# Performance work log

Measured on AMD Instinct MI355X. Metric: run time of the kernel, lower is better.

Reference implementation:

```python
import jax, jax.numpy as jnp
import numpy as np

L, H, D, F = 4, 8, 64, 256  # layers, heads, head_dim, FAVOR feature dims (n_dims=256 in source)
DM = H * D                   # d_model = 512
EPS = 1e-6                   # fast_transformers LinearAttention eps


def _ln(x, g, b):
    m = jnp.mean(x, -1, keepdims=True)
    v = jnp.mean((x - m) ** 2, -1, keepdims=True)
    return (x - m) * jax.lax.rsqrt(v + 1e-5) * g + b


def _favor(x, omega):
    # FAVOR+ softmax-kernel feature map. x: [B,S,H,D], omega: [D, F//2]
    x = x * (D ** -0.25)  # x * sqrt(softmax_temp), softmax_temp = 1/sqrt(D)
    u = jnp.einsum('bshd,df->bshf', x, omega)
    h = jnp.sum(x * x, -1, keepdims=True) * 0.5
    return jnp.concatenate([jnp.exp(u - h), jnp.exp(-u - h)], -1) * (F ** -0.5)


def _forward(x, pos, enc_w1, enc_b1, enc_w2, enc_b2, enc_g, enc_b,
             wq, bq, wk, bk, wv, bv, wo, bo, ln1_g, ln1_b,
             w1, b1, w2, b2, ln2_g, ln2_b, omega, cls_w, cls_b, num_graphs):
    B = num_graphs
    N = x.shape[0]
    S = N // B
    # encoder MLP + LayerNorm
    h = jnp.concatenate([x, pos], axis=1)
    h = jax.nn.relu(h @ enc_w1 + enc_b1)
    h = _ln(h @ enc_w2 + enc_b2, enc_g, enc_b)
    h = h.reshape(B, S, DM)
    # fast_transformers post-norm encoder layers with linear (FAVOR) attention
    for l in range(L):
        q = (h @ wq[l] + bq[l]).reshape(B, S, H, D)
        k = (h @ wk[l] + bk[l]).reshape(B, S, H, D)
        v = (h @ wv[l] + bv[l]).reshape(B, S, H, D)
        Q = _favor(q, omega[l])  # [B,S,H,F]
        K = _favor(k, omega[l])
        kv = jnp.einsum('bshf,bshd->bhfd', K, v)                      # associative accumulation
        z = 1.0 / (jnp.einsum('bshf,bhf->bsh', Q, K.sum(axis=1)) + EPS)
        a = jnp.einsum('bshf,bhfd,bsh->bshd', Q, kv, z).reshape(B, S, DM)
        h = _ln(h + a @ wo[l] + bo[l], ln1_g[l], ln1_b[l])            # x = norm1(x + attn)
        y = jax.nn.relu(h @ w1[l] + b1[l]) @ w2[l] + b2[l]            # FFN (relu)
        h = _ln(h + y, ln2_g[l], ln2_b[l])                            # norm2(x + y)
    pooled = h.mean(axis=1)
    return pooled @ cls_w + cls_b


def setup_inputs() -> dict:
    key = jax.random.key(0)
    ks = jax.random.split(key, 16)
    B, S = 16, 1024
    N = B * S

    def w(k, shape):
        return jax.random.normal(k, shape, jnp.float32) * 0.02

    return dict(
        x=jax.random.normal(ks[0], (N, 3), jnp.float32),
        pos=jax.random.normal(ks[1], (N, 3), jnp.float32),
        enc_w1=w(ks[2], (6, DM // 2)), enc_b1=jnp.zeros((DM // 2,), jnp.float32),
        enc_w2=w(ks[3], (DM // 2, DM)), enc_b2=jnp.zeros((DM,), jnp.float32),
        enc_g=jnp.ones((DM,), jnp.float32), enc_b=jnp.zeros((DM,), jnp.float32),
        wq=w(ks[4], (L, DM, DM)), bq=jnp.zeros((L, DM), jnp.float32),
        wk=w(ks[5], (L, DM, DM)), bk=jnp.zeros((L, DM), jnp.float32),
        wv=w(ks[6], (L, DM, DM)), bv=jnp.zeros((L, DM), jnp.float32),
        wo=w(ks[7], (L, DM, DM)), bo=jnp.zeros((L, DM), jnp.float32),
        ln1_g=jnp.ones((L, DM), jnp.float32), ln1_b=jnp.zeros((L, DM), jnp.float32),
        w1=w(ks[8], (L, DM, 2 * DM)), b1=jnp.zeros((L, 2 * DM), jnp.float32),
        w2=w(ks[9], (L, 2 * DM, DM)), b2=jnp.zeros((L, DM), jnp.float32),
        ln2_g=jnp.ones((L, DM), jnp.float32), ln2_b=jnp.zeros((L, DM), jnp.float32),
        omega=jax.random.normal(ks[10], (L, D, F // 2), jnp.float32),
        cls_w=w(ks[11], (DM, 16)), cls_b=jnp.zeros((16,), jnp.float32),
        num_graphs=B,
    )


def reference(x, pos, enc_w1, enc_b1, enc_w2, enc_b2, enc_g, enc_b,
              wq, bq, wk, bk, wv, bv, wo, bo, ln1_g, ln1_b,
              w1, b1, w2, b2, ln2_g, ln2_b, omega, cls_w, cls_b, num_graphs):
    return _forward(x, pos, enc_w1, enc_b1, enc_w2, enc_b2, enc_g, enc_b,
                    wq, bq, wk, bk, wv, bv, wo, bo, ln1_g, ln1_b,
                    w1, b1, w2, b2, ln2_g, ln2_b, omega, cls_w, cls_b, num_graphs)
```

## Files before the change

### kernel.cpp

```cpp
#include <hip/hip_runtime.h>
#include <hip/hip_bf16.h>
#include <math.h>

#define NTOK 16384
#define BATCH 16
#define SEQ 1024
#define DMODEL 512
#define NHEAD 8
#define HDIM 64
#define FDIM 256
#define BH_TOT 128
#define SCALE_QK 0.3535533905932738f
#define SCALE2 0.125f
#define FSCALE 0.0625f

typedef __bf16 bf16x8_t __attribute__((ext_vector_type(8)));
typedef float f32x4_t  __attribute__((ext_vector_type(4)));
typedef unsigned short u16x8 __attribute__((ext_vector_type(8)));
typedef unsigned short u16x4 __attribute__((ext_vector_type(4)));
typedef const __attribute__((address_space(1))) char* gas_t;
typedef __attribute__((address_space(3))) char* las_t;

__device__ __forceinline__ float b2f(unsigned short u) {
    union { unsigned int i; float f; } c; c.i = ((unsigned int)u) << 16; return c.f;
}
__device__ __forceinline__ unsigned short f2bu(float f) {
    __hip_bfloat16 h = __float2bfloat16(f);
    return *(unsigned short*)&h;
}
__device__ __forceinline__ bf16x8_t u2b8(u16x8 u) {
    union { u16x8 a; bf16x8_t b; } c; c.a = u; return c.b;
}

__global__ void zero_kernel(float* __restrict__ p, int n) {
    int i = blockIdx.x * 256 + threadIdx.x;
    if (i < n) p[i] = 0.f;
}

__global__ __launch_bounds__(256) void convT_batch_kernel(
    const float* __restrict__ W, unsigned short* __restrict__ Wt, int K, int N,
    size_t in_lstride, size_t out_lstride)
{
    int l = blockIdx.z;
    W  += (size_t)l * in_lstride;
    Wt += (size_t)l * out_lstride;
    __shared__ float tile[32][33];
    int k0 = blockIdx.y * 32, n0 = blockIdx.x * 32;
    int t = threadIdx.x;
    int r = t >> 3, c4 = (t & 7) * 4;
    float4 v = *(const float4*)(W + (size_t)(k0 + r) * N + n0 + c4);
    tile[r][c4 + 0] = v.x; tile[r][c4 + 1] = v.y;
    tile[r][c4 + 2] = v.z; tile[r][c4 + 3] = v.w;
    __syncthreads();
    ushort4 o;
    o.x = f2bu(tile[c4 + 0][r]); o.y = f2bu(tile[c4 + 1][r]);
    o.z = f2bu(tile[c4 + 2][r]); o.w = f2bu(tile[c4 + 3][r]);
    *(ushort4*)(Wt + (size_t)(n0 + r) * K + k0 + c4) = o;
}

__global__ __launch_bounds__(256) void omT_kernel(
    const float* __restrict__ om, unsigned short* __restrict__ omT)
{
    int i = blockIdx.x * 256 + threadIdx.x;
    int l = i >> 13, rem = i & 8191;
    int f = rem >> 6, d = rem & 63;
    omT[(size_t)l * 8192 + f * 64 + d] = f2bu(om[(size_t)l * 8192 + d * 128 + f] * SCALE_QK);
}

__global__ __launch_bounds__(256) void enc1_kernel(
    const float* __restrict__ x, const float* __restrict__ pos,
    const float* __restrict__ w1, const float* __restrict__ b1,
    unsigned short* __restrict__ mid)
{
    int row = blockIdx.x, t = threadIdx.x;
    __shared__ float in6[6];
    if (t < 3) in6[t] = x[row * 3 + t];
    else if (t < 6) in6[t] = pos[row * 3 + (t - 3)];
    __syncthreads();
    float acc = b1[t];
#pragma unroll
    for (int j = 0; j < 6; j++) acc += in6[j] * w1[j * 256 + t];
    mid[(size_t)row * 256 + t] = f2bu(fmaxf(acc, 0.f));
}

template<int RELU>
__global__ __launch_bounds__(256) void gemm_bf16_kernel(
    const unsigned short* __restrict__ A, const unsigned short* __restrict__ Bt,
    const float* __restrict__ bias, unsigned short* __restrict__ C,
    int M, int K, int Nc, int nx)
{
    __shared__ __align__(16) unsigned short As[128 * 32];
    __shared__ __align__(16) unsigned short Bs[128 * 32];
    const int tid = threadIdx.x;
    const int id = blockIdx.x;
    const int xcd = id & 7, slot = id >> 3;
    const int bm = ((slot / nx) * 8 + xcd) * 128;
    const int bn = (slot % nx) * 128;
    const int wave = tid >> 6, lane = tid & 63;
    const int wr = (wave >> 1) * 64, wc = (wave & 1) * 64;
    const int lm = lane & 15, lk = (lane >> 4) * 8;

    f32x4_t acc[4][4];
#pragma unroll
    for (int i = 0; i < 4; i++)
#pragma unroll
        for (int j = 0; j < 4; j++)
            acc[i][j] = (f32x4_t){0.f, 0.f, 0.f, 0.f};

    for (int k0 = 0; k0 < K; k0 += 32) {
#pragma unroll
        for (int it = 0; it < 2; ++it) {
            int t = tid + it * 256;
            const unsigned short* gp = A + (size_t)(bm + (t >> 2)) * K + k0 + (t & 3) * 8;
            __builtin_amdgcn_global_load_lds((gas_t)(const char*)gp,
                (las_t)((char*)As + t * 16), 16, 0, 0);
        }
#pragma unroll
        for (int it = 0; it < 2; ++it) {
            int t = tid + it * 256;
            const unsigned short* gp = Bt + (size_t)(bn + (t >> 2)) * K + k0 + (t & 3) * 8;
            __builtin_amdgcn_global_load_lds((gas_t)(const char*)gp,
                (las_t)((char*)Bs + t * 16), 16, 0, 0);
        }
        __syncthreads();
        bf16x8_t af[4], bfr[4];
#pragma unroll
        for (int i = 0; i < 4; i++)
            af[i] = *(const bf16x8_t*)(As + (size_t)(wr + 16 * i + lm) * 32 + lk);
#pragma unroll
        for (int j = 0; j < 4; j++)
            bfr[j] = *(const bf16x8_t*)(Bs + (size_t)(wc + 16 * j + lm) * 32 + lk);
#pragma unroll
        for (int i = 0; i < 4; i++)
#pragma unroll
            for (int j = 0; j < 4; j++)
                acc[i][j] = __builtin_amdgcn_mfma_f32_16x16x32_bf16(af[i], bfr[j], acc[i][j], 0, 0, 0);
        __syncthreads();
    }

    const int col_l = lane & 15;
    const int row_q = (lane >> 4) * 4;
#pragma unroll
    for (int i = 0; i < 4; i++) {
#pragma unroll
        for (int j = 0; j < 4; j++) {
            int gn = bn + wc + 16 * j + col_l;
            float bsv = bias[gn];
            int gm0 = bm + wr + 16 * i + row_q;
#pragma unroll
            for (int r = 0; r < 4; r++) {
                float v = acc[i][j][r] + bsv;
                if (RELU) v = fmaxf(v, 0.f);
                C[(size_t)(gm0 + r) * Nc + gn] = f2bu(v);
            }
        }
    }
}

__global__ __launch_bounds__(256) void gemm_qkv_kernel(
    const unsigned short* __restrict__ A, const unsigned short* __restrict__ Bt,
    const float* __restrict__ bq, const float* __restrict__ bk, const float* __restrict__ bv,
    unsigned short* __restrict__ Q, unsigned short* __restrict__ Kk,
    unsigned short* __restrict__ vT)
{
    __shared__ __align__(16) unsigned short As[128 * 32];
    __shared__ __align__(16) unsigned short Bs[128 * 32];
    const int tid = threadIdx.x;
    const int id = blockIdx.x;
    const int xcd = id & 7, slot = id >> 3;
    const int bm = ((slot / 12) * 8 + xcd) * 128;
    const int bn = (slot % 12) * 128;
    const int wave = tid >> 6, lane = tid & 63;
    const int wr = (wave >> 1) * 64, wc = (wave & 1) * 64;
    const int lm = lane & 15, lk = (lane >> 4) * 8;
    const int K = DMODEL;

    f32x4_t acc[4][4];
#pragma unroll
    for (int i = 0; i < 4; i++)
#pragma unroll
        for (int j = 0; j < 4; j++)
            acc[i][j] = (f32x4_t){0.f, 0.f, 0.f, 0.f};

    for (int k0 = 0; k0 < K; k0 += 32) {
#pragma unroll
        for (int it = 0; it < 2; ++it) {
            int t = tid + it * 256;
            const unsigned short* gp = A + (size_t)(bm + (t >> 2)) * K + k0 + (t & 3) * 8;
            __builtin_amdgcn_global_load_lds((gas_t)(const char*)gp,
                (las_t)((char*)As + t * 16), 16, 0, 0);
        }
#pragma unroll
        for (int it = 0; it < 2; ++it) {
            int t = tid + it * 256;
            const unsigned short* gp = Bt + (size_t)(bn + (t >> 2)) * K + k0 + (t & 3) * 8;
            __builtin_amdgcn_global_load_lds((gas_t)(const char*)gp,
                (las_t)((char*)Bs + t * 16), 16, 0, 0);
        }
        __syncthreads();
        bf16x8_t af[4], bfr[4];
#pragma unroll
        for (int i = 0; i < 4; i++)
            af[i] = *(const bf16x8_t*)(As + (size_t)(wr + 16 * i + lm) * 32 + lk);
#pragma unroll
        for (int j = 0; j < 4; j++)
            bfr[j] = *(const bf16x8_t*)(Bs + (size_t)(wc + 16 * j + lm) * 32 + lk);
#pragma unroll
        for (int i = 0; i < 4; i++)
#pragma unroll
            for (int j = 0; j < 4; j++)
                acc[i][j] = __builtin_amdgcn_mfma_f32_16x16x32_bf16(af[i], bfr[j], acc[i][j], 0, 0, 0);
        __syncthreads();
    }

    const int sect = bn >> 9;
    const float* bias = (sect == 0) ? bq : (sect == 1) ? bk : bv;
    unsigned short* rowout = (sect == 0) ? Q : Kk;
    const int cb = bn & 511;
    const int col_l = lane & 15;
    const int row_q = (lane >> 4) * 4;
#pragma unroll
    for (int i = 0; i < 4; i++) {
#pragma unroll
        for (int j = 0; j < 4; j++) {
            int cn = cb + wc + 16 * j + col_l;
            float bsv = bias[cn];
            int gm0 = bm + wr + 16 * i + row_q;
            if (sect < 2) {
#pragma unroll
                for (int r = 0; r < 4; r++)
                    rowout[(size_t)(gm0 + r) * DMODEL + cn] = f2bu(acc[i][j][r] + bsv);
            } else {
                int bb_ = gm0 >> 10, ss = gm0 & 1023;
                int hh_ = cn >> 6, dd = cn & 63;
                u16x4 o4;
#pragma unroll
                for (int r = 0; r < 4; r++) o4[r] = f2bu(acc[i][j][r] + bsv);
                *(u16x4*)(vT + (((size_t)(bb_ * NHEAD + hh_) * HDIM + dd) * SEQ + ss)) = o4;
            }
        }
    }
}

__global__ __launch_bounds__(256) void favor_k_kv_kernel(
    const unsigned short* __restrict__ Kx,
    const unsigned short* __restrict__ vT,
    const unsigned short* __restrict__ omT,
    float* __restrict__ kvpart,
    float* __restrict__ ksum)
{
    const int bid = blockIdx.x;
    const int chunk = bid & 3;
    const int bh = bid >> 2;
    const int b = bh >> 3, h = bh & 7;
    const int tid = threadIdx.x;
    const int wave = tid >> 6, lane = tid & 63;
    const int lm = lane & 15, q = lane >> 4, lk = q * 8;
    const int quad4 = q * 4;
    const int wr = wave * 64;
    const int m0 = wave * 16;

    __shared__ __align__(16) unsigned short phiT[256 * 72];

    f32x4_t acc_kv[4][4];
#pragma unroll
    for (int i = 0; i < 4; i++)
#pragma unroll
        for (int j = 0; j < 4; j++)
            acc_kv[i][j] = (f32x4_t){0.f, 0.f, 0.f, 0.f};
    float ks_acc = 0.f;

    const unsigned short* vbase = vT + (size_t)bh * HDIM * SEQ;

    for (int st = 0; st < 4; ++st) {
        int s0 = chunk * 256 + st * 64;
        const unsigned short* krow = Kx + (size_t)(b * SEQ + s0 + m0 + lm) * DMODEL + h * HDIM;
        u16x8 xu0 = *(const u16x8*)(krow + lk);
        u16x8 xu1 = *(const u16x8*)(krow + 32 + lk);
        float p = 0.f;
#pragma unroll
        for (int e = 0; e < 8; e++) {
            float a = b2f(xu0[e]), c = b2f(xu1[e]);
            p += a * a + c * c;
        }
        p += __shfl_xor(p, 16, 64);
        p += __shfl_xor(p, 32, 64);
        float hred = 0.5f * SCALE2 * p;
        float hr[4];
#pragma unroll
        for (int r = 0; r < 4; r++) hr[r] = __shfl(hred, quad4 + r, 64);
        f32x4_t acc[8];
#pragma unroll
        for (int j = 0; j < 8; j++) acc[j] = (f32x4_t){0.f, 0.f, 0.f, 0.f};
        bf16x8_t af0 = u2b8(xu0), af1 = u2b8(xu1);
#pragma unroll
        for (int j = 0; j < 8; j++) {
            bf16x8_t b0 = *(const bf16x8_t*)(omT + (size_t)(j * 16 + lm) * 64 + lk);
            acc[j] = __builtin_amdgcn_mfma_f32_16x16x32_bf16(af0, b0, acc[j], 0, 0, 0);
            bf16x8_t b1 = *(const bf16x8_t*)(omT + (size_t)(j * 16 + lm) * 64 + 32 + lk);
            acc[j] = __builtin_amdgcn_mfma_f32_16x16x32_bf16(af1, b1, acc[j], 0, 0, 0);
        }
        __syncthreads();
#pragma unroll
        for (int j = 0; j < 8; j++) {
            int f = j * 16 + lm;
#pragma unroll
            for (int r = 0; r < 4; r++) {
                int m = m0 + quad4 + r;
                float u = acc[j][r];
                phiT[f * 72 + m]         = f2bu(__expf(u - hr[r]) * FSCALE);
                phiT[(f + 128) * 72 + m] = f2bu(__expf(-u - hr[r]) * FSCALE);
            }
        }
        __syncthreads();
        {
            const unsigned short* row = &phiT[tid * 72];
#pragma unroll
            for (int mm = 0; mm < 64; mm += 8) {
                u16x8 v = *(const u16x8*)(row + mm);
#pragma unroll
                for (int e = 0; e < 8; e++) ks_acc += b2f(v[e]);
            }
        }
#pragma unroll
        for (int ks = 0; ks < 2; ks++) {
            bf16x8_t af[4], bfr[4];
#pragma unroll
            for (int i = 0; i < 4; i++)
                af[i] = *(const bf16x8_t*)&phiT[(wr + 16 * i + lm) * 72 + ks * 32 + lk];
#pragma unroll
            for (int j = 0; j < 4; j++)
                bfr[j] = *(const bf16x8_t*)(vbase + (size_t)(16 * j + lm) * SEQ + s0 + ks * 32 + lk);
#pragma unroll
            for (int i = 0; i < 4; i++)
#pragma unroll
                for (int j = 0; j < 4; j++)
                    acc_kv[i][j] = __builtin_amdgcn_mfma_f32_16x16x32_bf16(af[i], bfr[j], acc_kv[i][j], 0, 0, 0);
        }
    }

    float* kp = kvpart + ((size_t)chunk * BH_TOT + bh) * HDIM * FDIM;
#pragma unroll
    for (int i = 0; i < 4; i++) {
#pragma unroll
        for (int j = 0; j < 4; j++) {
            int d = 16 * j + lm;
            int f0 = wr + 16 * i + quad4;
            *(f32x4_t*)(kp + (size_t)d * FDIM + f0) = acc_kv[i][j];
        }
    }
    atomicAdd(&ksum[(size_t)bh * FDIM + tid], ks_acc);
}

__global__ __launch_bounds__(256) void reduce_kv_kernel(
    const float* __restrict__ in, unsigned short* __restrict__ out)
{
    const size_t STRIDE = (size_t)BH_TOT * HDIM * FDIM;
    size_t i = (size_t)blockIdx.x * 256 + threadIdx.x;
    out[i] = f2bu(in[i] + in[i + STRIDE] + in[i + 2 * STRIDE] + in[i + 3 * STRIDE]);
}

__global__ __launch_bounds__(256) void favor_q_attn_kernel(
    const unsigned short* __restrict__ Qx,
    const unsigned short* __restrict__ omT,
    const unsigned short* __restrict__ kvT,
    const float* __restrict__ ksum,
    unsigned short* __restrict__ outX)
{
    const int bid = blockIdx.x;
    const int sc = bid & 15;
    const int bh = bid >> 4;
    const int b = bh >> 3, h = bh & 7;
    const int s0 = sc * 64;
    const int tid = threadIdx.x;
    const int wave = tid >> 6, lane = tid & 63;
    const int lm = lane & 15, q = lane >> 4, lk = q * 8;
    const int quad4 = q * 4;
    const int m0 = wave * 16;

    __shared__ __align__(16) unsigned short phis[4][16 * 136];
    __shared__ __align__(16) float kss[4][256];

    *(float4*)&kss[wave][lane * 4] = *(const float4*)(ksum + (size_t)bh * FDIM + lane * 4);

    const unsigned short* qrow = Qx + (size_t)(b * SEQ + s0 + m0 + lm) * DMODEL + h * HDIM;
    u16x8 xu0 = *(const u16x8*)(qrow + lk);
    u16x8 xu1 = *(const u16x8*)(qrow + 32 + lk);
    float p = 0.f;
#pragma unroll
    for (int e = 0; e < 8; e++) {
        float a = b2f(xu0[e]), c = b2f(xu1[e]);
        p += a * a + c * c;
    }
    p += __shfl_xor(p, 16, 64);
    p += __shfl_xor(p, 32, 64);
    float hred = 0.5f * SCALE2 * p;
    float hr[4];
#pragma unroll
    for (int r = 0; r < 4; r++) hr[r] = __shfl(hred, quad4 + r, 64);

    f32x4_t acc[8];
#pragma unroll
    for (int j = 0; j < 8; j++) acc[j] = (f32x4_t){0.f, 0.f, 0.f, 0.f};
    bf16x8_t af0 = u2b8(xu0), af1 = u2b8(xu1);
#pragma unroll
    for (int j = 0; j < 8; j++) {
        bf16x8_t b0 = *(const bf16x8_t*)(omT + (size_t)(j * 16 + lm) * 64 + lk);
        acc[j] = __builtin_amdgcn_mfma_f32_16x16x32_bf16(af0, b0, acc[j], 0, 0, 0);
        bf16x8_t b1 = *(const bf16x8_t*)(omT + (size_t)(j * 16 + lm) * 64 + 32 + lk);
        acc[j] = __builtin_amdgcn_mfma_f32_16x16x32_bf16(af1, b1, acc[j], 0, 0, 0);
    }

    unsigned short* ph = phis[wave];
    float zp[4] = {0.f, 0.f, 0.f, 0.f};
#pragma unroll
    for (int j = 0; j < 8; j++) {
        int f = j * 16 + lm;
        float ksp = kss[wave][f], ksm = kss[wave][128 + f];
#pragma unroll
        for (int r = 0; r < 4; r++) {
            float u = acc[j][r];
            float pp = __expf(u - hr[r]) * FSCALE;
            float pm = __expf(-u - hr[r]) * FSCALE;
            ph[(quad4 + r) * 136 + f] = f2bu(pp);
            zp[r] += pp * ksp + pm * ksm;
        }
    }
#pragma unroll
    for (int off = 1; off < 16; off <<= 1) {
        zp[0] += __shfl_xor(zp[0], off, 64);
        zp[1] += __shfl_xor(zp[1], off, 64);
        zp[2] += __shfl_xor(zp[2], off, 64);
        zp[3] += __shfl_xor(zp[3], off, 64);
    }
    float zinv[4];
#pragma unroll
    for (int r = 0; r < 4; r++) zinv[r] = 1.f / (zp[r] + 1e-6f);

    const unsigned short* kvbase = kvT + (size_t)bh * HDIM * FDIM;
    f32x4_t acc_o[4];
#pragma unroll
    for (int j = 0; j < 4; j++) acc_o[j] = (f32x4_t){0.f, 0.f, 0.f, 0.f};
#pragma unroll
    for (int k0 = 0; k0 < 128; k0 += 32) {
        bf16x8_t af = *(const bf16x8_t*)&ph[lm * 136 + k0 + lk];
#pragma unroll
        for (int j = 0; j < 4; j++) {
            bf16x8_t bfr = *(const bf16x8_t*)(kvbase + (size_t)(16 * j + lm) * FDIM + k0 + lk);
            acc_o[j] = __builtin_amdgcn_mfma_f32_16x16x32_bf16(af, bfr, acc_o[j], 0, 0, 0);
        }
    }
#pragma unroll
    for (int j = 0; j < 8; j++) {
        int f = j * 16 + lm;
#pragma unroll
        for (int r = 0; r < 4; r++)
            ph[(quad4 + r) * 136 + f] = f2bu(__expf(-acc[j][r] - hr[r]) * FSCALE);
    }
#pragma unroll
    for (int k0 = 0; k0 < 128; k0 += 32) {
        bf16x8_t af = *(const bf16x8_t*)&ph[lm * 136 + k0 + lk];
#pragma unroll
        for (int j = 0; j < 4; j++) {
            bf16x8_t bfr = *(const bf16x8_t*)(kvbase + (size_t)(16 * j + lm) * FDIM + 128 + k0 + lk);
            acc_o[j] = __builtin_amdgcn_mfma_f32_16x16x32_bf16(af, bfr, acc_o[j], 0, 0, 0);
        }
    }
#pragma unroll
    for (int r = 0; r < 4; r++) {
        int s = s0 + m0 + quad4 + r;
#pragma unroll
        for (int j = 0; j < 4; j++) {
            int d = 16 * j + lm;
            outX[(size_t)(b * SEQ + s) * DMODEL + h * HDIM + d] = f2bu(acc_o[j][r] * zinv[r]);
        }
    }
}

template<int HAS_RES>
__global__ __launch_bounds__(512) void add_ln_kernel(
    const unsigned short* __restrict__ res16, const unsigned short* __restrict__ tin16,
    const float* __restrict__ g, const float* __restrict__ bb,
    unsigned short* __restrict__ out16)
{
    int row = blockIdx.x, t = threadIdx.x;
    size_t idx = (size_t)row * DMODEL + t;
    float val = b2f(tin16[idx]);
    if (HAS_RES) val += b2f(res16[idx]);
    float s1 = val, s2 = val * val;
#pragma unroll
    for (int off = 32; off; off >>= 1) {
        s1 += __shfl_down(s1, off, 64);
        s2 += __shfl_down(s2, off, 64);
    }
    __shared__ float w1s[8], w2s[8];
    int wid = t >> 6, lane = t & 63;
    if (lane == 0) { w1s[wid] = s1; w2s[wid] = s2; }
    __syncthreads();
    if (t == 0) {
        float a1 = 0.f, a2 = 0.f;
#pragma unroll
        for (int i = 0; i < 8; i++) { a1 += w1s[i]; a2 += w2s[i]; }
        w1s[0] = a1 * (1.f / DMODEL);
        w2s[0] = a2 * (1.f / DMODEL);
    }
    __syncthreads();
    float m = w1s[0];
    float var = w2s[0] - m * m;
    float r = rsqrtf(var + 1e-5f);
    out16[idx] = f2bu((val - m) * r * g[t] + bb[t]);
}

__global__ __launch_bounds__(256) void pool_part_kernel(
    const unsigned short* __restrict__ h16, float* __restrict__ pbuf)
{
    int blk = blockIdx.x;
    int b = blk >> 4, ch = blk & 15;
    int t = threadIdx.x;
    int d0 = t * 2;
    float a0 = 0.f, a1 = 0.f;
    const unsigned short* base = h16 + ((size_t)(b * SEQ + ch * 64) * DMODEL) + d0;
#pragma unroll 4
    for (int s = 0; s < 64; s++) {
        ushort2 v = *(const ushort2*)(base + (size_t)s * DMODEL);
        a0 += b2f(v.x); a1 += b2f(v.y);
    }
    *(float2*)(pbuf + (size_t)blk * DMODEL + d0) = make_float2(a0, a1);
}

__global__ __launch_bounds__(512) void cls_kernel(
    const float* __restrict__ pbuf, const float* __restrict__ cls_w,
    const float* __restrict__ cls_b, float* __restrict__ out)
{
    int b = blockIdx.x, t = threadIdx.x;
    float s = 0.f;
#pragma unroll
    for (int c = 0; c < 16; c++) s += pbuf[(size_t)(b * 16 + c) * DMODEL + t];
    __shared__ float pooled[DMODEL];
    pooled[t] = s * (1.f / SEQ);
    __syncthreads();
    if (t < 16) {
        float acc = cls_b[t];
        for (int c = 0; c < DMODEL; c++) acc += pooled[c] * cls_w[c * 16 + t];
        out[b * 16 + t] = acc;
    }
}

extern "C" void kernel_launch(void* const* d_in, const int* in_sizes, int n_in,
                              void* d_out, int out_size, void* d_ws, size_t ws_size,
                              hipStream_t stream)
{
    const float* x      = (const float*)d_in[0];
    const float* pos    = (const float*)d_in[1];
    const float* enc_w1 = (const float*)d_in[2];
    const float* enc_b1 = (const float*)d_in[3];
    const float* enc_w2 = (const float*)d_in[4];
    const float* enc_b2 = (const float*)d_in[5];
    const float* enc_g  = (const float*)d_in[6];
    const float* enc_bb = (const float*)d_in[7];
    const float* wq = (const float*)d_in[8];
    const float* bq = (const float*)d_in[9];
    const float* wk = (const float*)d_in[10];
    const float* bk = (const float*)d_in[11];
    const float* wv = (const float*)d_in[12];
    const float* bv = (const float*)d_in[13];
    const float* wo = (const float*)d_in[14];
    const float* bo = (const float*)d_in[15];
    const float* ln1_g = (const float*)d_in[16];
    const float* ln1_b = (const float*)d_in[17];
    const float* w1 = (const float*)d_in[18];
    const float* b1 = (const float*)d_in[19];
    const float* w2 = (const float*)d_in[20];
    const float* b2 = (const float*)d_in[21];
    const float* ln2_g = (const float*)d_in[22];
    const float* ln2_b = (const float*)d_in[23];
    const float* omega = (const float*)d_in[24];
    const float* cls_w = (const float*)d_in[25];
    const float* cls_b = (const float*)d_in[26];
    float* out = (float*)d_out;

    const int N = NTOK;
    const int BH = BH_TOT;

    char* p = (char*)d_ws;
    unsigned short* qb16 = (unsigned short*)p; p += (size_t)N * DMODEL * 2;
    unsigned short* kb16 = (unsigned short*)p; p += (size_t)N * DMODEL * 2;
    unsigned short* vT16 = (unsigned short*)p; p += (size_t)N * DMODEL * 2;
    unsigned short* h16  = (unsigned short*)p; p += (size_t)N * DMODEL * 2;
    unsigned short* mid16 = (unsigned short*)p; p += (size_t)N * 1024 * 2;
    unsigned short* attn16 = (unsigned short*)p; p += (size_t)N * DMODEL * 2;
    float* kvpart = (float*)p;                 p += (size_t)4 * BH * HDIM * FDIM * 4;
    unsigned short* kvT16 = (unsigned short*)p; p += (size_t)BH * HDIM * FDIM * 2;
    float* ksb = (float*)p;                    p += (size_t)BH * FDIM * 4;
    float* pbuf = (float*)p;                   p += (size_t)BATCH * 16 * DMODEL * 4;
    unsigned short* enc_w2t = (unsigned short*)p; p += (size_t)256 * 512 * 2;
    unsigned short* wqkvt = (unsigned short*)p; p += (size_t)4 * 1536 * 512 * 2;
    unsigned short* wot = (unsigned short*)p;  p += (size_t)4 * 512 * 512 * 2;
    unsigned short* w1t = (unsigned short*)p;  p += (size_t)4 * 512 * 1024 * 2;
    unsigned short* w2t = (unsigned short*)p;  p += (size_t)4 * 1024 * 512 * 2;
    unsigned short* omT = (unsigned short*)p;  p += (size_t)4 * 128 * 64 * 2;

    convT_batch_kernel<<<dim3(16, 8, 1), 256, 0, stream>>>(enc_w2, enc_w2t, 256, 512, 0, 0);
    convT_batch_kernel<<<dim3(16, 16, 4), 256, 0, stream>>>(wq, wqkvt,            512, 512, 262144, 786432);
    convT_batch_kernel<<<dim3(16, 16, 4), 256, 0, stream>>>(wk, wqkvt + 262144,   512, 512, 262144, 786432);
    convT_batch_kernel<<<dim3(16, 16, 4), 256, 0, stream>>>(wv, wqkvt + 524288,   512, 512, 262144, 786432);
    convT_batch_kernel<<<dim3(16, 16, 4), 256, 0, stream>>>(wo, wot, 512, 512, 262144, 262144);
    convT_batch_kernel<<<dim3(32, 16, 4), 256, 0, stream>>>(w1, w1t, 512, 1024, 524288, 524288);
    convT_batch_kernel<<<dim3(16, 32, 4), 256, 0, stream>>>(w2, w2t, 1024, 512, 524288, 524288);
    omT_kernel<<<128, 256, 0, stream>>>(omega, omT);

    enc1_kernel<<<N, 256, 0, stream>>>(x, pos, enc_w1, enc_b1, mid16);
    gemm_bf16_kernel<0><<<4 * 128, 256, 0, stream>>>(mid16, enc_w2t, enc_b2, qb16, N, 256, 512, 4);
    add_ln_kernel<0><<<N, 512, 0, stream>>>(nullptr, qb16, enc_g, enc_bb, h16);

    for (int l = 0; l < 4; l++) {
        const unsigned short* omT_l = omT + (size_t)l * 8192;
        gemm_qkv_kernel<<<12 * 128, 256, 0, stream>>>(
            h16, wqkvt + (size_t)l * 786432,
            bq + l * DMODEL, bk + l * DMODEL, bv + l * DMODEL,
            qb16, kb16, vT16);
        zero_kernel<<<BH * FDIM / 256, 256, 0, stream>>>(ksb, BH * FDIM);
        favor_k_kv_kernel<<<BH * 4, 256, 0, stream>>>(kb16, vT16, omT_l, kvpart, ksb);
        reduce_kv_kernel<<<BH * HDIM * FDIM / 256, 256, 0, stream>>>(kvpart, kvT16);
        favor_q_attn_kernel<<<BH * 16, 256, 0, stream>>>(qb16, omT_l, kvT16, ksb, attn16);
        gemm_bf16_kernel<0><<<4 * 128, 256, 0, stream>>>(attn16, wot + (size_t)l * 262144, bo + l * DMODEL, qb16, N, 512, 512, 4);
        add_ln_kernel<1><<<N, 512, 0, stream>>>(h16, qb16, ln1_g + l * DMODEL, ln1_b + l * DMODEL, h16);
        gemm_bf16_kernel<1><<<8 * 128, 256, 0, stream>>>(h16, w1t + (size_t)l * 524288, b1 + l * 1024, mid16, N, 512, 1024, 8);
        gemm_bf16_kernel<0><<<4 * 128, 256, 0, stream>>>(mid16, w2t + (size_t)l * 524288, b2 + l * DMODEL, qb16, N, 1024, 512, 4);
        add_ln_kernel<1><<<N, 512, 0, stream>>>(h16, qb16, ln2_g + l * DMODEL, ln2_b + l * DMODEL, h16);
    }

    pool_part_kernel<<<BATCH * 16, 256, 0, stream>>>(h16, pbuf);
    cls_kernel<<<BATCH, 512, 0, stream>>>(pbuf, cls_w, cls_b, out);
}
```

Baseline: 1.225 ms.

## Drop ksum atomics, remap FAVOR blocks by XCD, cache phi-minus, batch encoder rows

Several small changes land together. The ksum zero kernel and its atomics are replaced by per-chunk partial sums that the existing kv reduce kernel also reduces, which removes one launch per layer. Block indices in both FAVOR kernels are remapped so blocks sharing a batch-head land on the same XCD for L2 locality. The q-attention kernel keeps ksum in registers and stores the packed phi-minus values from the first pass instead of recomputing the exponentials. The first encoder kernel processes 8 rows per block with weights held in registers, at the cost of some extra register pressure.

```diff
diff --git a/kernel.cpp b/kernel.cpp
--- a/kernel.cpp
+++ b/kernel.cpp
@@ -30,11 +30,6 @@
 }
 __device__ __forceinline__ bf16x8_t u2b8(u16x8 u) {
     union { u16x8 a; bf16x8_t b; } c; c.a = u; return c.b;
-}
-
-__global__ void zero_kernel(float* __restrict__ p, int n) {
-    int i = blockIdx.x * 256 + threadIdx.x;
-    if (i < n) p[i] = 0.f;
 }
 
 __global__ __launch_bounds__(256) void convT_batch_kernel(
@@ -72,15 +67,20 @@
     const float* __restrict__ w1, const float* __restrict__ b1,
     unsigned short* __restrict__ mid)
 {
-    int row = blockIdx.x, t = threadIdx.x;
-    __shared__ float in6[6];
-    if (t < 3) in6[t] = x[row * 3 + t];
-    else if (t < 6) in6[t] = pos[row * 3 + (t - 3)];
-    __syncthreads();
-    float acc = b1[t];
-#pragma unroll
-    for (int j = 0; j < 6; j++) acc += in6[j] * w1[j * 256 + t];
-    mid[(size_t)row * 256 + t] = f2bu(fmaxf(acc, 0.f));
+    int t = threadIdx.x;
+    int row0 = blockIdx.x * 8;
+    float w[6];
+#pragma unroll
+    for (int j = 0; j < 6; j++) w[j] = w1[j * 256 + t];
+    float bias = b1[t];
+#pragma unroll
+    for (int rr = 0; rr < 8; rr++) {
+        int row = row0 + rr;
+        float acc = bias
+            + x[row * 3 + 0] * w[0] + x[row * 3 + 1] * w[1] + x[row * 3 + 2] * w[2]
+            + pos[row * 3 + 0] * w[3] + pos[row * 3 + 1] * w[4] + pos[row * 3 + 2] * w[5];
+        mid[(size_t)row * 256 + t] = f2bu(fmaxf(acc, 0.f));
+    }
 }
 
 template<int RELU>
@@ -247,11 +247,12 @@
     const unsigned short* __restrict__ vT,
     const unsigned short* __restrict__ omT,
     float* __restrict__ kvpart,
-    float* __restrict__ ksum)
+    float* __restrict__ kspart)
 {
     const int bid = blockIdx.x;
-    const int chunk = bid & 3;
-    const int bh = bid >> 2;
+    const int xcd = bid & 7, slot = bid >> 3;
+    const int chunk = slot & 3;
+    const int bh = (slot >> 2) * 8 + xcd;
     const int b = bh >> 3, h = bh & 7;
     const int tid = threadIdx.x;
     const int wave = tid >> 6, lane = tid & 63;
@@ -349,15 +350,22 @@
             *(f32x4_t*)(kp + (size_t)d * FDIM + f0) = acc_kv[i][j];
         }
     }
-    atomicAdd(&ksum[(size_t)bh * FDIM + tid], ks_acc);
+    kspart[(size_t)chunk * (BH_TOT * FDIM) + (size_t)bh * FDIM + tid] = ks_acc;
 }
 
 __global__ __launch_bounds__(256) void reduce_kv_kernel(
-    const float* __restrict__ in, unsigned short* __restrict__ out)
-{
-    const size_t STRIDE = (size_t)BH_TOT * HDIM * FDIM;
-    size_t i = (size_t)blockIdx.x * 256 + threadIdx.x;
-    out[i] = f2bu(in[i] + in[i + STRIDE] + in[i + 2 * STRIDE] + in[i + 3 * STRIDE]);
+    const float* __restrict__ in_kv, const float* __restrict__ in_ks,
+    unsigned short* __restrict__ out_kv, float* __restrict__ out_ks)
+{
+    const int NKV = BH_TOT * HDIM * FDIM;
+    const int NKS = BH_TOT * FDIM;
+    int i = blockIdx.x * 256 + threadIdx.x;
+    if (i < NKV) {
+        out_kv[i] = f2bu(in_kv[i] + in_kv[i + NKV] + in_kv[i + 2 * NKV] + in_kv[i + 3 * NKV]);
+    } else {
+        int j = i - NKV;
+        out_ks[j] = in_ks[j] + in_ks[j + NKS] + in_ks[j + 2 * NKS] + in_ks[j + 3 * NKS];
+    }
 }
 
 __global__ __launch_bounds__(256) void favor_q_attn_kernel(
@@ -368,8 +376,9 @@
     unsigned short* __restrict__ outX)
 {
     const int bid = blockIdx.x;
-    const int sc = bid & 15;
-    const int bh = bid >> 4;
+    const int xcd = bid & 7, slot = bid >> 3;
+    const int sc = slot & 15;
+    const int bh = (slot >> 4) * 8 + xcd;
     const int b = bh >> 3, h = bh & 7;
     const int s0 = sc * 64;
     const int tid = threadIdx.x;
@@ -379,9 +388,14 @@
     const int m0 = wave * 16;
 
     __shared__ __align__(16) unsigned short phis[4][16 * 136];
-    __shared__ __align__(16) float kss[4][256];
-
-    *(float4*)&kss[wave][lane * 4] = *(const float4*)(ksum + (size_t)bh * FDIM + lane * 4);
+
+    const float* ksb = ksum + (size_t)bh * FDIM;
+    float ksp[8], ksm[8];
+#pragma unroll
+    for (int j = 0; j < 8; j++) {
+        ksp[j] = ksb[j * 16 + lm];
+        ksm[j] = ksb[128 + j * 16 + lm];
+    }
 
     const unsigned short* qrow = Qx + (size_t)(b * SEQ + s0 + m0 + lm) * DMODEL + h * HDIM;
     u16x8 xu0 = *(const u16x8*)(qrow + lk);
@@ -412,18 +426,23 @@
     }
 
     unsigned short* ph = phis[wave];
+    unsigned int pm[8][2];
     float zp[4] = {0.f, 0.f, 0.f, 0.f};
 #pragma unroll
     for (int j = 0; j < 8; j++) {
         int f = j * 16 + lm;
-        float ksp = kss[wave][f], ksm = kss[wave][128 + f];
 #pragma unroll
         for (int r = 0; r < 4; r++) {
             float u = acc[j][r];
             float pp = __expf(u - hr[r]) * FSCALE;
-            float pm = __expf(-u - hr[r]) * FSCALE;
+            float pmv = __expf(-u - hr[r]) * FSCALE;
             ph[(quad4 + r) * 136 + f] = f2bu(pp);
-            zp[r] += pp * ksp + pm * ksm;
+            unsigned short pmu = f2bu(pmv);
+            if (r == 0)      pm[j][0] = pmu;
+            else if (r == 1) pm[j][0] |= ((unsigned int)pmu << 16);
+            else if (r == 2) pm[j][1] = pmu;
+            else             pm[j][1] |= ((unsigned int)pmu << 16);
+            zp[r] += pp * ksp[j] + pmv * ksm[j];
         }
     }
 #pragma unroll
@@ -453,9 +472,10 @@
 #pragma unroll
     for (int j = 0; j < 8; j++) {
         int f = j * 16 + lm;
-#pragma unroll
-        for (int r = 0; r < 4; r++)
-            ph[(quad4 + r) * 136 + f] = f2bu(__expf(-acc[j][r] - hr[r]) * FSCALE);
+        ph[(quad4 + 0) * 136 + f] = (unsigned short)(pm[j][0] & 0xffffu);
+        ph[(quad4 + 1) * 136 + f] = (unsigned short)(pm[j][0] >> 16);
+        ph[(quad4 + 2) * 136 + f] = (unsigned short)(pm[j][1] & 0xffffu);
+        ph[(quad4 + 3) * 136 + f] = (unsigned short)(pm[j][1] >> 16);
     }
 #pragma unroll
     for (int k0 = 0; k0 < 128; k0 += 32) {
@@ -590,6 +610,7 @@
     unsigned short* mid16 = (unsigned short*)p; p += (size_t)N * 1024 * 2;
     unsigned short* attn16 = (unsigned short*)p; p += (size_t)N * DMODEL * 2;
     float* kvpart = (float*)p;                 p += (size_t)4 * BH * HDIM * FDIM * 4;
+    float* kspart = (float*)p;                 p += (size_t)4 * BH * FDIM * 4;
     unsigned short* kvT16 = (unsigned short*)p; p += (size_t)BH * HDIM * FDIM * 2;
     float* ksb = (float*)p;                    p += (size_t)BH * FDIM * 4;
     float* pbuf = (float*)p;                   p += (size_t)BATCH * 16 * DMODEL * 4;
@@ -609,19 +630,19 @@
     convT_batch_kernel<<<dim3(16, 32, 4), 256, 0, stream>>>(w2, w2t, 1024, 512, 524288, 524288);
     omT_kernel<<<128, 256, 0, stream>>>(omega, omT);
 
-    enc1_kernel<<<N, 256, 0, stream>>>(x, pos, enc_w1, enc_b1, mid16);
+    enc1_kernel<<<N / 8, 256, 0, stream>>>(x, pos, enc_w1, enc_b1, mid16);
     gemm_bf16_kernel<0><<<4 * 128, 256, 0, stream>>>(mid16, enc_w2t, enc_b2, qb16, N, 256, 512, 4);
     add_ln_kernel<0><<<N, 512, 0, stream>>>(nullptr, qb16, enc_g, enc_bb, h16);
 
+    const int RED_BLOCKS = (BH * HDIM * FDIM + BH * FDIM) / 256;
     for (int l = 0; l < 4; l++) {
         const unsigned short* omT_l = omT + (size_t)l * 8192;
         gemm_qkv_kernel<<<12 * 128, 256, 0, stream>>>(
             h16, wqkvt + (size_t)l * 786432,
             bq + l * DMODEL, bk + l * DMODEL, bv + l * DMODEL,
             qb16, kb16, vT16);
-        zero_kernel<<<BH * FDIM / 256, 256, 0, stream>>>(ksb, BH * FDIM);
-        favor_k_kv_kernel<<<BH * 4, 256, 0, stream>>>(kb16, vT16, omT_l, kvpart, ksb);
-        reduce_kv_kernel<<<BH * HDIM * FDIM / 256, 256, 0, stream>>>(kvpart, kvT16);
+        favor_k_kv_kernel<<<BH * 4, 256, 0, stream>>>(kb16, vT16, omT_l, kvpart, kspart);
+        reduce_kv_kernel<<<RED_BLOCKS, 256, 0, stream>>>(kvpart, kspart, kvT16, ksb);
         favor_q_attn_kernel<<<BH * 16, 256, 0, stream>>>(qb16, omT_l, kvT16, ksb, attn16);
         gemm_bf16_kernel<0><<<4 * 128, 256, 0, stream>>>(attn16, wot + (size_t)l * 262144, bo + l * DMODEL, qb16, N, 512, 512, 4);
         add_ln_kernel<1><<<N, 512, 0, stream>>>(h16, qb16, ln1_g + l * DMODEL, ln1_b + l * DMODEL, h16);
```

Measured after the change: 1.196 ms. -2.4%, faster.
